# Performance work log

Hardware: AMD Instinct MI355X
Metric: run time of the kernel (lower is better)

Reference implementation:

```python
import jax, jax.numpy as jnp
import numpy as np

V, BLK, D, H, L = 50257, 2048, 768, 12, 4
HD = D // H
EPS = 1e-5


def _ln(x, w, b):
    mu = jnp.mean(x, axis=-1, keepdims=True)
    var = jnp.mean(jnp.square(x - mu), axis=-1, keepdims=True)
    return (x - mu) * jax.lax.rsqrt(var + EPS) * w + b


def setup_inputs() -> dict:
    key = jax.random.key(0)
    ks = iter(jax.random.split(key, 32))
    s = 0.02
    idx = jax.random.randint(next(ks), (2, 2048), 0, V)
    inp = {
        "idx": idx,
        "wte": jax.random.normal(next(ks), (V, D), jnp.float32) * s,
        "wpe": jax.random.normal(next(ks), (BLK, D), jnp.float32) * s,
        # stacked per-layer params [L, ...]
        "ln1_w": jnp.ones((L, D), jnp.float32),
        "ln1_b": jnp.zeros((L, D), jnp.float32),
        "attn_w": jax.random.normal(next(ks), (L, D, 3 * D), jnp.float32) * s,
        "attn_b": jnp.zeros((L, 3 * D), jnp.float32),
        "proj_w": jax.random.normal(next(ks), (L, D, D), jnp.float32) * (s / np.sqrt(2 * L)),
        "proj_b": jnp.zeros((L, D), jnp.float32),
        "ln2_w": jnp.ones((L, D), jnp.float32),
        "ln2_b": jnp.zeros((L, D), jnp.float32),
        "fc_w": jax.random.normal(next(ks), (L, D, 4 * D), jnp.float32) * s,
        "fc_b": jnp.zeros((L, 4 * D), jnp.float32),
        "fcp_w": jax.random.normal(next(ks), (L, 4 * D, D), jnp.float32) * (s / np.sqrt(2 * L)),
        "fcp_b": jnp.zeros((L, D), jnp.float32),
        "lnf_w": jnp.ones((D,), jnp.float32),
        "lnf_b": jnp.zeros((D,), jnp.float32),
    }
    return inp


def _gpt_forward(idx, wte, wpe, ln1_w, ln1_b, attn_w, attn_b, proj_w, proj_b,
                 ln2_w, ln2_b, fc_w, fc_b, fcp_w, fcp_b, lnf_w, lnf_b):
    B, T = idx.shape
    x = wte[idx] + wpe[:T]  # [B,T,D]; dropout p=0 -> identity
    causal = jnp.tril(jnp.ones((T, T), bool))
    scale = 1.0 / np.sqrt(HD)

    def block(x, p):
        l1w, l1b, aw, ab, pw, pb, l2w, l2b, fw, fb, fpw, fpb = p
        h = _ln(x, l1w, l1b)
        qkv = h @ aw + ab  # [B,T,3D]
        q, k, v = jnp.split(qkv, 3, axis=-1)
        q = q.reshape(B, T, H, HD).transpose(0, 2, 1, 3)  # [B,H,T,hd]
        k = k.reshape(B, T, H, HD).transpose(0, 2, 1, 3)
        v = v.reshape(B, T, H, HD).transpose(0, 2, 1, 3)
        att = jnp.einsum('bhqd,bhkd->bhqk', q, k) * scale
        att = jnp.where(causal, att, -jnp.inf)
        att = jax.nn.softmax(att, axis=-1)
        y = jnp.einsum('bhqk,bhkd->bhqd', att, v)
        y = y.transpose(0, 2, 1, 3).reshape(B, T, D)
        x = x + y @ pw + pb
        h2 = _ln(x, l2w, l2b)
        m = jax.nn.gelu(h2 @ fw + fb, approximate=False) @ fpw + fpb
        return x + m, None

    params = (ln1_w, ln1_b, attn_w, attn_b, proj_w, proj_b,
              ln2_w, ln2_b, fc_w, fc_b, fcp_w, fcp_b)
    x, _ = jax.lax.scan(block, x, params)
    x = _ln(x, lnf_w, lnf_b)
    # inference path: logits only for last position, lm_head tied to wte
    logits = x[:, -1:, :] @ wte.T  # [B,1,V]
    return logits


def reference(idx, wte, wpe, ln1_w, ln1_b, attn_w, attn_b, proj_w, proj_b,
              ln2_w, ln2_b, fc_w, fc_b, fcp_w, fcp_b, lnf_w, lnf_b):
    return _gpt_forward(idx, wte, wpe, ln1_w, ln1_b, attn_w, attn_b, proj_w, proj_b,
                        ln2_w, ln2_b, fc_w, fc_b, fcp_w, fcp_b, lnf_w, lnf_b)
```

## Files before the change

kernel.cpp:

```cpp
#include <hip/hip_runtime.h>
#include <math.h>

#define V 50257
#define B 2
#define T 2048
#define D 768
#define H 12
#define HD 64
#define L 4
#define D3 (3*D)
#define D4 (4*D)
#define NTOK (B*T)
#define EPS 1e-5f

typedef __bf16 v8bf __attribute__((ext_vector_type(8)));
typedef __bf16 v4bf __attribute__((ext_vector_type(4)));
typedef unsigned short v8us __attribute__((ext_vector_type(8)));
typedef float  v4f  __attribute__((ext_vector_type(4)));

#define GAS(p) ((const __attribute__((address_space(1))) void*)(p))
#define LAS(p) ((__attribute__((address_space(3))) void*)(p))

#define LIDX(row, chunk) ((row)*64 + ((((chunk) ^ ((row)&7)))<<3))
#define CIDX(row, chunk) ((row)*128 + ((((chunk) ^ ((row)&7)))<<3))

__global__ __launch_bounds__(256) void prep_kernel(
        const int* __restrict__ idx, const float* __restrict__ wte,
        const float* __restrict__ wpe, float* __restrict__ x,
        const float* __restrict__ aw_all,  const float* __restrict__ pw_all,
        const float* __restrict__ fw_all,  const float* __restrict__ fpw_all,
        __bf16* __restrict__ awt_all, __bf16* __restrict__ pwt_all,
        __bf16* __restrict__ fwt_all, __bf16* __restrict__ fpwt_all) {
    int bid = blockIdx.x;
    if (bid < 3072) {
        int e = (bid * 256 + threadIdx.x) * 4;
        int pos = e / D;
        int d   = e - pos * D;
        int t   = pos & (T - 1);
        int tok = idx[pos];
        const float4 a  = *(const float4*)(wte + (size_t)tok * D + d);
        const float4 p4 = *(const float4*)(wpe + (size_t)t * D + d);
        float4 r; r.x = a.x + p4.x; r.y = a.y + p4.y; r.z = a.z + p4.z; r.w = a.w + p4.w;
        *(float4*)(x + e) = r;
        return;
    }
    bid -= 3072;
    const int l = bid / 6912; bid -= l * 6912;
    const float* W; __bf16* Wt; int K, N, bx, by;
    if (bid < 1728)      {             W = aw_all  + (size_t)l * D  * D3; Wt = awt_all  + (size_t)l * D3 * D;  K = D;  N = D3; bx = bid % 72; by = bid / 72; }
    else if (bid < 2304) { bid -= 1728; W = pw_all  + (size_t)l * D  * D;  Wt = pwt_all  + (size_t)l * D  * D;  K = D;  N = D;  bx = bid % 24; by = bid / 24; }
    else if (bid < 4608) { bid -= 2304; W = fw_all  + (size_t)l * D  * D4; Wt = fwt_all  + (size_t)l * D4 * D;  K = D;  N = D4; bx = bid % 96; by = bid / 96; }
    else                 { bid -= 4608; W = fpw_all + (size_t)l * D4 * D;  Wt = fpwt_all + (size_t)l * D  * D4; K = D4; N = D;  bx = bid % 24; by = bid / 24; }
    __shared__ float t[32][33];
    const int n0 = bx * 32, k0 = by * 32;
    const int tx = threadIdx.x & 31, ty = threadIdx.x >> 5;
    #pragma unroll
    for (int p = 0; p < 4; ++p)
        t[ty + 8 * p][tx] = W[(size_t)(k0 + ty + 8 * p) * N + n0 + tx];
    __syncthreads();
    #pragma unroll
    for (int p = 0; p < 4; ++p)
        Wt[(size_t)(n0 + ty + 8 * p) * K + k0 + tx] = (__bf16)t[tx][ty + 8 * p];
}

__global__ __launch_bounds__(256) void ln_kernel(const float* __restrict__ X,
                                                 const float* __restrict__ w,
                                                 const float* __restrict__ b,
                                                 __bf16* __restrict__ Y,
                                                 int src_mul, int src_off) {
    int srow = blockIdx.x * src_mul + src_off;
    const float* xr = X + (size_t)srow * D;
    float v[3];
    float s = 0.f, s2 = 0.f;
    #pragma unroll
    for (int j = 0; j < 3; ++j) {
        v[j] = xr[threadIdx.x + 256 * j];
        s += v[j];
        s2 += v[j] * v[j];
    }
    #pragma unroll
    for (int off = 32; off; off >>= 1) {
        s  += __shfl_xor(s, off);
        s2 += __shfl_xor(s2, off);
    }
    __shared__ float ss[4], ss2[4];
    int wave = threadIdx.x >> 6, lane = threadIdx.x & 63;
    if (lane == 0) { ss[wave] = s; ss2[wave] = s2; }
    __syncthreads();
    s  = ss[0] + ss[1] + ss[2] + ss[3];
    s2 = ss2[0] + ss2[1] + ss2[2] + ss2[3];
    float mu  = s * (1.f / D);
    float var = s2 * (1.f / D) - mu * mu;
    float rs  = rsqrtf(var + EPS);
    __bf16* yr = Y + (size_t)blockIdx.x * D;
    #pragma unroll
    for (int j = 0; j < 3; ++j) {
        int c = threadIdx.x + 256 * j;
        yr[c] = (__bf16)((v[j] - mu) * rs * w[c] + b[c]);
    }
}

template<bool DOGELU>
__global__ __launch_bounds__(256) void gemm_bt(const __bf16* __restrict__ A,
                                               const __bf16* __restrict__ Wt,
                                               const float* __restrict__ bias,
                                               __bf16* __restrict__ Cout,
                                               int N, int K) {
    __shared__ __align__(16) __bf16 sm[16384];
    __bf16* As = sm;
    __bf16* Bs = sm + 8192;
    const int tid  = threadIdx.x;
    const int w    = tid >> 6;
    const int lane = tid & 63;
    const int row0 = blockIdx.y * 128;
    const int col0 = blockIdx.x * 128;

    const int srow = ((tid >> 6) & 3) * 16 + (tid & 15);
    const int sk   = ((tid >> 4) & 3) * 8;
    const __bf16* gA0 = A  + (size_t)(row0 + srow) * K + sk;
    const __bf16* gA1 = gA0 + (size_t)64 * K;
    const __bf16* gB0 = Wt + (size_t)(col0 + srow) * K + sk;
    const __bf16* gB1 = gB0 + (size_t)64 * K;
    __bf16* lA0 = As + (size_t)tid * 8;
    __bf16* lA1 = As + (size_t)(tid + 256) * 8;
    __bf16* lB0 = Bs + (size_t)tid * 8;
    __bf16* lB1 = Bs + (size_t)(tid + 256) * 8;

    const int wr = w >> 1, wc = w & 1;
    const __bf16* rA = As + wr * 2048 + lane * 8;
    const __bf16* rB = Bs + wc * 2048 + lane * 8;

    __builtin_amdgcn_global_load_lds(GAS(gA0), LAS(lA0), 16, 0, 0);
    __builtin_amdgcn_global_load_lds(GAS(gA1), LAS(lA1), 16, 0, 0);
    __builtin_amdgcn_global_load_lds(GAS(gB0), LAS(lB0), 16, 0, 0);
    __builtin_amdgcn_global_load_lds(GAS(gB1), LAS(lB1), 16, 0, 0);
    gA0 += 32; gA1 += 32; gB0 += 32; gB1 += 32;
    __syncthreads();

    v4f acc[4][4] = {};
    const int nt = K >> 5;
    for (int t = 0; t < nt; ++t) {
        const int cb = (t & 1) * 4096;
        if (t + 1 < nt) {
            const int nb = ((t + 1) & 1) * 4096;
            __builtin_amdgcn_global_load_lds(GAS(gA0), LAS(lA0 + nb), 16, 0, 0);
            __builtin_amdgcn_global_load_lds(GAS(gA1), LAS(lA1 + nb), 16, 0, 0);
            __builtin_amdgcn_global_load_lds(GAS(gB0), LAS(lB0 + nb), 16, 0, 0);
            __builtin_amdgcn_global_load_lds(GAS(gB1), LAS(lB1 + nb), 16, 0, 0);
            gA0 += 32; gA1 += 32; gB0 += 32; gB1 += 32;
        }
        v8bf af[4], bfr[4];
        #pragma unroll
        for (int i = 0; i < 4; ++i) af[i]  = *(const v8bf*)(rA + cb + i * 512);
        #pragma unroll
        for (int j = 0; j < 4; ++j) bfr[j] = *(const v8bf*)(rB + cb + j * 512);
        #pragma unroll
        for (int i = 0; i < 4; ++i)
            #pragma unroll
            for (int j = 0; j < 4; ++j)
                acc[i][j] = __builtin_amdgcn_mfma_f32_16x16x32_bf16(af[i], bfr[j], acc[i][j], 0, 0, 0);
        __syncthreads();
    }

    const int er = (lane >> 4) * 4;
    const int ec = lane & 15;
    #pragma unroll
    for (int j = 0; j < 4; ++j) {
        const int col = wc * 64 + j * 16 + ec;
        const float bval = bias[col0 + col];
        const int chunk = col >> 3, ce = col & 7;
        #pragma unroll
        for (int i = 0; i < 4; ++i) {
            const int rowb = wr * 64 + i * 16 + er;
            #pragma unroll
            for (int rr = 0; rr < 4; ++rr) {
                float vv = acc[i][j][rr] + bval;
                if (DOGELU) vv = 0.5f * vv * (1.f + erff(vv * 0.70710678118f));
                sm[CIDX(rowb + rr, chunk) + ce] = (__bf16)vv;
            }
        }
    }
    __syncthreads();
    #pragma unroll
    for (int c = 0; c < 8; ++c) {
        const int chunkid = tid + c * 256;
        const int row = chunkid >> 4;
        const int cc  = chunkid & 15;
        *(v8us*)(void*)(Cout + (size_t)(row0 + row) * N + col0 + cc * 8) =
            *(const v8us*)(const void*)(sm + CIDX(row, cc));
    }
}

__global__ __launch_bounds__(256) void gemm64(const __bf16* __restrict__ A,
                                              const __bf16* __restrict__ Wt,
                                              const float* __restrict__ bias,
                                              const float* __restrict__ res,
                                              float* __restrict__ Cout,
                                              int N, int K) {
    __shared__ __align__(16) __bf16 sm[16384];
    __bf16* As = sm;
    __bf16* Bs = sm + 8192;
    const int tid  = threadIdx.x;
    const int w    = tid >> 6;
    const int lane = tid & 63;
    const int row0 = blockIdx.y * 64;
    const int col0 = blockIdx.x * 64;

    const int srow = ((tid >> 7) & 3) * 16 + (tid & 15);
    const int sk   = ((tid >> 4) & 7) * 8;
    const __bf16* gA0 = A  + (size_t)(row0 + srow) * K + sk;
    const __bf16* gA1 = gA0 + (size_t)32 * K;
    const __bf16* gB0 = Wt + (size_t)(col0 + srow) * K + sk;
    const __bf16* gB1 = gB0 + (size_t)32 * K;
    __bf16* lA0 = As + (size_t)tid * 8;
    __bf16* lA1 = As + (size_t)(tid + 256) * 8;
    __bf16* lB0 = Bs + (size_t)tid * 8;
    __bf16* lB1 = Bs + (size_t)(tid + 256) * 8;

    const int wr = w >> 1, wc = w & 1;
    const __bf16* rA = As + wr * 2048 + lane * 8;
    const __bf16* rB = Bs + wc * 2048 + lane * 8;

    __builtin_amdgcn_global_load_lds(GAS(gA0), LAS(lA0), 16, 0, 0);
    __builtin_amdgcn_global_load_lds(GAS(gA1), LAS(lA1), 16, 0, 0);
    __builtin_amdgcn_global_load_lds(GAS(gB0), LAS(lB0), 16, 0, 0);
    __builtin_amdgcn_global_load_lds(GAS(gB1), LAS(lB1), 16, 0, 0);
    gA0 += 64; gA1 += 64; gB0 += 64; gB1 += 64;
    __syncthreads();

    v4f acc[2][2] = {};
    const int nt = K >> 6;
    for (int t = 0; t < nt; ++t) {
        const int cb = (t & 1) * 4096;
        if (t + 1 < nt) {
            const int nb = ((t + 1) & 1) * 4096;
            __builtin_amdgcn_global_load_lds(GAS(gA0), LAS(lA0 + nb), 16, 0, 0);
            __builtin_amdgcn_global_load_lds(GAS(gA1), LAS(lA1 + nb), 16, 0, 0);
            __builtin_amdgcn_global_load_lds(GAS(gB0), LAS(lB0 + nb), 16, 0, 0);
            __builtin_amdgcn_global_load_lds(GAS(gB1), LAS(lB1 + nb), 16, 0, 0);
            gA0 += 64; gA1 += 64; gB0 += 64; gB1 += 64;
        }
        #pragma unroll
        for (int h = 0; h < 2; ++h) {
            v8bf af[2], bfr[2];
            #pragma unroll
            for (int i = 0; i < 2; ++i) af[i]  = *(const v8bf*)(rA + cb + i * 1024 + h * 512);
            #pragma unroll
            for (int j = 0; j < 2; ++j) bfr[j] = *(const v8bf*)(rB + cb + j * 1024 + h * 512);
            #pragma unroll
            for (int i = 0; i < 2; ++i)
                #pragma unroll
                for (int j = 0; j < 2; ++j)
                    acc[i][j] = __builtin_amdgcn_mfma_f32_16x16x32_bf16(af[i], bfr[j], acc[i][j], 0, 0, 0);
        }
        __syncthreads();
    }

    const int er = (lane >> 4) * 4;
    const int ec = lane & 15;
    #pragma unroll
    for (int j = 0; j < 2; ++j) {
        const int col = col0 + wc * 32 + j * 16 + ec;
        const float bval = bias[col];
        #pragma unroll
        for (int i = 0; i < 2; ++i) {
            #pragma unroll
            for (int rr = 0; rr < 4; ++rr) {
                const int row = row0 + wr * 32 + i * 16 + er + rr;
                Cout[(size_t)row * N + col] = acc[i][j][rr] + bval + res[(size_t)row * N + col];
            }
        }
    }
}

__global__ __launch_bounds__(256) void attn_mfma(const __bf16* __restrict__ qkv,
                                                 __bf16* __restrict__ y) {
    __shared__ __align__(16) __bf16 Qs[4096];
    __shared__ __align__(16) __bf16 Ks[4096];
    __shared__ __align__(16) __bf16 Vt[4096];
    __shared__ __align__(16) __bf16 Ps[4][1024];

    const int tid  = threadIdx.x;
    const int w    = tid >> 6;
    const int lane = tid & 63;
    const int quad = lane >> 4;
    const int l4   = lane & 15;

    const int qt = 31 - (blockIdx.x & 31);
    const int bh = blockIdx.x >> 5;
    const int b  = bh / H;
    const int h  = bh - b * H;
    const int q0 = qt * 64;

    const __bf16* base = qkv + (size_t)(b * T) * D3 + h * HD;

    {
        int c = tid;
        #pragma unroll
        for (int rep = 0; rep < 2; ++rep, c += 256) {
            int row = c >> 3, ch = c & 7;
            v8us v = *(const v8us*)(const void*)(base + (size_t)(q0 + row) * D3 + ch * 8);
            *(v8us*)(void*)(Qs + LIDX(row, ch)) = v;
        }
    }

    const int krow = tid >> 3, kch = tid & 7;
    const int vkp = tid & 31, vdc = tid >> 5;
    const __bf16* kp0 = base + D     + (size_t)krow * D3 + kch * 8;
    const __bf16* kp1 = kp0 + (size_t)32 * D3;
    const __bf16* vp0 = base + 2 * D + (size_t)(2 * vkp) * D3 + vdc * 8;
    const __bf16* vp1 = vp0 + D3;

    v8us kr0 = *(const v8us*)(const void*)kp0;
    v8us kr1 = *(const v8us*)(const void*)kp1;
    v8us vr0 = *(const v8us*)(const void*)vp0;
    v8us vr1 = *(const v8us*)(const void*)vp1;

    float m_local = -INFINITY;
    v4f o[4] = {};
    v4f sacc = {};
    v8bf qf[2];
    v8bf vones;
    #pragma unroll
    for (int i = 0; i < 8; ++i) vones[i] = (__bf16)1.0f;

    const int nt = qt + 1;
    const size_t adv = (size_t)64 * D3;
    const int qrow = q0 + w * 16 + l4;

    for (int kt = 0; kt < nt; ++kt) {
        const int k0 = kt * 64;
        *(v8us*)(void*)(Ks + LIDX(krow, kch))      = kr0;
        *(v8us*)(void*)(Ks + LIDX(krow + 32, kch)) = kr1;
        #pragma unroll
        for (int j = 0; j < 8; ++j) {
            int dim = vdc * 8 + j;
            int idx = dim * 64 + ((((vkp >> 2) ^ (dim & 7))) << 3) + ((vkp & 3) << 1);
            *(unsigned int*)(void*)(Vt + idx) =
                ((unsigned int)vr1[j] << 16) | (unsigned int)vr0[j];
        }
        __syncthreads();

        if (kt == 0) {
            #pragma unroll
            for (int kh = 0; kh < 2; ++kh)
                qf[kh] = *(const v8bf*)(Qs + LIDX(w * 16 + l4, kh * 4 + quad));
        }
        if (kt + 1 < nt) {
            kp0 += adv; kp1 += adv; vp0 += adv; vp1 += adv;
            kr0 = *(const v8us*)(const void*)kp0;
            kr1 = *(const v8us*)(const void*)kp1;
            vr0 = *(const v8us*)(const void*)vp0;
            vr1 = *(const v8us*)(const void*)vp1;
        }

        v4f s[4] = {};
        __builtin_amdgcn_s_setprio(1);
        #pragma unroll
        for (int kh = 0; kh < 2; ++kh) {
            #pragma unroll
            for (int jb = 0; jb < 4; ++jb) {
                v8bf bk = *(const v8bf*)(Ks + LIDX(jb * 16 + l4, kh * 4 + quad));
                s[jb] = __builtin_amdgcn_mfma_f32_16x16x32_bf16(bk, qf[kh], s[jb], 0, 0, 0);
            }
        }
        __builtin_amdgcn_s_setprio(0);

        float sv[4][4];
        float mx = -INFINITY;
        #pragma unroll
        for (int jb = 0; jb < 4; ++jb) {
            #pragma unroll
            for (int rg = 0; rg < 4; ++rg) {
                float vvv = s[jb][rg] * 0.125f;
                if (k0 + jb * 16 + quad * 4 + rg > qrow) vvv = -INFINITY;
                sv[jb][rg] = vvv;
                mx = fmaxf(mx, vvv);
            }
        }
        mx = fmaxf(mx, __shfl_xor(mx, 16));
        mx = fmaxf(mx, __shfl_xor(mx, 32));
        if (!__all(mx <= m_local + 8.f)) {
            const float mnew    = fmaxf(m_local, mx);
            const float alpha_l = __expf(m_local - mnew);
            m_local = mnew;
            float a4[4];
            #pragma unroll
            for (int r = 0; r < 4; ++r) a4[r] = __shfl(alpha_l, quad * 4 + r);
            #pragma unroll
            for (int r = 0; r < 4; ++r) {
                sacc[r] *= a4[r];
                #pragma unroll
                for (int db = 0; db < 4; ++db) o[db][r] *= a4[r];
            }
        }
        #pragma unroll
        for (int jb = 0; jb < 4; ++jb) {
            v4bf pk;
            #pragma unroll
            for (int rg = 0; rg < 4; ++rg)
                pk[rg] = (__bf16)__expf(sv[jb][rg] - m_local);
            *(v4bf*)(void*)(&Ps[w][LIDX(l4, jb * 2 + (quad >> 1)) + ((quad & 1) << 2)]) = pk;
        }
        __builtin_amdgcn_s_setprio(1);
        #pragma unroll
        for (int kh = 0; kh < 2; ++kh) {
            v8bf ap = *(const v8bf*)(&Ps[w][LIDX(l4, kh * 4 + quad)]);
            sacc = __builtin_amdgcn_mfma_f32_16x16x32_bf16(ap, vones, sacc, 0, 0, 0);
            #pragma unroll
            for (int db = 0; db < 4; ++db) {
                v8bf bv = *(const v8bf*)(Vt + LIDX(db * 16 + l4, kh * 4 + quad));
                o[db] = __builtin_amdgcn_mfma_f32_16x16x32_bf16(ap, bv, o[db], 0, 0, 0);
            }
        }
        __builtin_amdgcn_s_setprio(0);
        __syncthreads();
    }

    #pragma unroll
    for (int db = 0; db < 4; ++db) {
        #pragma unroll
        for (int r = 0; r < 4; ++r) {
            const int q = q0 + w * 16 + quad * 4 + r;
            y[(size_t)(b * T + q) * D + h * HD + db * 16 + l4] =
                (__bf16)(o[db][r] / sacc[r]);
        }
    }
}

__global__ __launch_bounds__(256) void logits_kernel(const __bf16* __restrict__ xf,
                                                     const float* __restrict__ wte,
                                                     float* __restrict__ out) {
    int wave = threadIdx.x >> 6;
    int lane = threadIdx.x & 63;
    int v = blockIdx.x * 4 + wave;
    if (v >= V) return;
    const float4* wr = (const float4*)(wte + (size_t)v * D);
    const v4bf*   x0 = (const v4bf*)(xf);
    const v4bf*   x1 = (const v4bf*)(xf + D);
    float s0 = 0.f, s1 = 0.f;
    #pragma unroll
    for (int j = 0; j < 3; ++j) {
        float4 wv = wr[lane + 64 * j];
        v4bf a0 = x0[lane + 64 * j];
        v4bf a1 = x1[lane + 64 * j];
        s0 = fmaf(wv.x, (float)a0[0], s0); s0 = fmaf(wv.y, (float)a0[1], s0);
        s0 = fmaf(wv.z, (float)a0[2], s0); s0 = fmaf(wv.w, (float)a0[3], s0);
        s1 = fmaf(wv.x, (float)a1[0], s1); s1 = fmaf(wv.y, (float)a1[1], s1);
        s1 = fmaf(wv.z, (float)a1[2], s1); s1 = fmaf(wv.w, (float)a1[3], s1);
    }
    #pragma unroll
    for (int off = 32; off; off >>= 1) {
        s0 += __shfl_xor(s0, off);
        s1 += __shfl_xor(s1, off);
    }
    if (lane == 0) { out[v] = s0; out[V + v] = s1; }
}

extern "C" void kernel_launch(void* const* d_in, const int* in_sizes, int n_in,
                              void* d_out, int out_size, void* d_ws, size_t ws_size,
                              hipStream_t stream) {
    const int*   idx    = (const int*)  d_in[0];
    const float* wte    = (const float*)d_in[1];
    const float* wpe    = (const float*)d_in[2];
    const float* ln1_w  = (const float*)d_in[3];
    const float* ln1_b  = (const float*)d_in[4];
    const float* attn_w = (const float*)d_in[5];
    const float* attn_b = (const float*)d_in[6];
    const float* proj_w = (const float*)d_in[7];
    const float* proj_b = (const float*)d_in[8];
    const float* ln2_w  = (const float*)d_in[9];
    const float* ln2_b  = (const float*)d_in[10];
    const float* fc_w   = (const float*)d_in[11];
    const float* fc_b   = (const float*)d_in[12];
    const float* fcp_w  = (const float*)d_in[13];
    const float* fcp_b  = (const float*)d_in[14];
    const float* lnf_w  = (const float*)d_in[15];
    const float* lnf_b  = (const float*)d_in[16];
    float* out = (float*)d_out;

    char* ws = (char*)d_ws;
    float*  x    = (float*)ws;  ws += (size_t)NTOK * D  * 4;
    __bf16* qkvb = (__bf16*)ws;
    __bf16* gb   = (__bf16*)ws; ws += (size_t)NTOK * D4 * 2;
    __bf16* hb   = (__bf16*)ws; ws += (size_t)NTOK * D  * 2;
    __bf16* yb   = (__bf16*)ws; ws += (size_t)NTOK * D  * 2;
    __bf16* awt  = (__bf16*)ws; ws += (size_t)L * D3 * D   * 2;
    __bf16* pwt  = (__bf16*)ws; ws += (size_t)L * D  * D   * 2;
    __bf16* fwt  = (__bf16*)ws; ws += (size_t)L * D4 * D   * 2;
    __bf16* fpwt = (__bf16*)ws; ws += (size_t)L * D  * D4  * 2;
    __bf16* xf   = (__bf16*)ws; ws += (size_t)B * D    * 2;

    prep_kernel<<<3072 + 6912 * L, 256, 0, stream>>>(idx, wte, wpe, x,
                                                     attn_w, proj_w, fc_w, fcp_w,
                                                     awt, pwt, fwt, fpwt);

    for (int l = 0; l < L; ++l) {
        const float* l1w = ln1_w + l * D;
        const float* l1b = ln1_b + l * D;
        const float* ab  = attn_b + l * D3;
        const float* pb  = proj_b + l * D;
        const float* l2w = ln2_w + l * D;
        const float* l2b = ln2_b + l * D;
        const float* fb  = fc_b + l * D4;
        const float* fpb = fcp_b + l * D;
        const __bf16* awl  = awt  + (size_t)l * D3 * D;
        const __bf16* pwl  = pwt  + (size_t)l * D  * D;
        const __bf16* fwl  = fwt  + (size_t)l * D4 * D;
        const __bf16* fpwl = fpwt + (size_t)l * D  * D4;

        ln_kernel<<<NTOK, 256, 0, stream>>>(x, l1w, l1b, hb, 1, 0);
        gemm_bt<false><<<dim3(D3 / 128, NTOK / 128), 256, 0, stream>>>(
            hb, awl, ab, qkvb, D3, D);
        attn_mfma<<<B * H * (T / 64), 256, 0, stream>>>(qkvb, yb);
        gemm64<<<dim3(D / 64, NTOK / 64), 256, 0, stream>>>(
            yb, pwl, pb, x, x, D, D);
        ln_kernel<<<NTOK, 256, 0, stream>>>(x, l2w, l2b, hb, 1, 0);
        gemm_bt<true><<<dim3(D4 / 128, NTOK / 128), 256, 0, stream>>>(
            hb, fwl, fb, gb, D4, D);
        gemm64<<<dim3(D / 64, NTOK / 64), 256, 0, stream>>>(
            gb, fpwl, fpb, x, x, D, D4);
    }

    ln_kernel<<<B, 256, 0, stream>>>(x, lnf_w, lnf_b, xf, T, T - 1);
    logits_kernel<<<(V + 3) / 4, 256, 0, stream>>>(xf, wte, out);
}
```

Baseline: 1.286 ms.

## Triple-buffer GEMM loads, remap workgroups across XCDs, vectorize residual epilogue

Both GEMM kernels move from double to triple-buffered LDS staging, with explicit vmcnt waits and raw s_barriers so global-to-LDS loads run two tiles ahead. Workgroup IDs in the GEMMs and attention are permuted so consecutive tiles land on the same XCD, which is meant to improve L2 reuse. The gemm64 epilogue now stages results in swizzled LDS and writes float4 with coalesced residual reads. The cost is 1.5x LDS per block, which may reduce occupancy, plus correctness risk from the hand-written waitcnt counts.

```diff
diff --git a/kernel.cpp b/kernel.cpp
--- a/kernel.cpp
+++ b/kernel.cpp
@@ -23,6 +23,8 @@
 
 #define LIDX(row, chunk) ((row)*64 + ((((chunk) ^ ((row)&7)))<<3))
 #define CIDX(row, chunk) ((row)*128 + ((((chunk) ^ ((row)&7)))<<3))
+
+#define SBAR() asm volatile("s_barrier" ::: "memory")
 
 __global__ __launch_bounds__(256) void prep_kernel(
         const int* __restrict__ idx, const float* __restrict__ wte,
@@ -106,14 +108,16 @@
                                                const float* __restrict__ bias,
                                                __bf16* __restrict__ Cout,
                                                int N, int K) {
-    __shared__ __align__(16) __bf16 sm[16384];
-    __bf16* As = sm;
-    __bf16* Bs = sm + 8192;
+    __shared__ __align__(16) __bf16 sm[24576];
     const int tid  = threadIdx.x;
     const int w    = tid >> 6;
     const int lane = tid & 63;
-    const int row0 = blockIdx.y * 128;
-    const int col0 = blockIdx.x * 128;
+
+    int fid = blockIdx.y * gridDim.x + blockIdx.x;
+    const int nwg = gridDim.x * gridDim.y;
+    fid = (fid & 7) * (nwg >> 3) + (fid >> 3);
+    const int row0 = (fid / gridDim.x) * 128;
+    const int col0 = (fid % gridDim.x) * 128;
 
     const int srow = ((tid >> 6) & 3) * 16 + (tid & 15);
     const int sk   = ((tid >> 4) & 3) * 8;
@@ -121,33 +125,33 @@
     const __bf16* gA1 = gA0 + (size_t)64 * K;
     const __bf16* gB0 = Wt + (size_t)(col0 + srow) * K + sk;
     const __bf16* gB1 = gB0 + (size_t)64 * K;
-    __bf16* lA0 = As + (size_t)tid * 8;
-    __bf16* lA1 = As + (size_t)(tid + 256) * 8;
-    __bf16* lB0 = Bs + (size_t)tid * 8;
-    __bf16* lB1 = Bs + (size_t)(tid + 256) * 8;
+
+    auto stage = [&](int bsel) {
+        __bf16* dst = sm + bsel * 8192;
+        __builtin_amdgcn_global_load_lds(GAS(gA0), LAS(dst + (size_t)tid * 8), 16, 0, 0);
+        __builtin_amdgcn_global_load_lds(GAS(gA1), LAS(dst + (size_t)(tid + 256) * 8), 16, 0, 0);
+        __builtin_amdgcn_global_load_lds(GAS(gB0), LAS(dst + 4096 + (size_t)tid * 8), 16, 0, 0);
+        __builtin_amdgcn_global_load_lds(GAS(gB1), LAS(dst + 4096 + (size_t)(tid + 256) * 8), 16, 0, 0);
+        gA0 += 32; gA1 += 32; gB0 += 32; gB1 += 32;
+    };
 
     const int wr = w >> 1, wc = w & 1;
-    const __bf16* rA = As + wr * 2048 + lane * 8;
-    const __bf16* rB = Bs + wc * 2048 + lane * 8;
-
-    __builtin_amdgcn_global_load_lds(GAS(gA0), LAS(lA0), 16, 0, 0);
-    __builtin_amdgcn_global_load_lds(GAS(gA1), LAS(lA1), 16, 0, 0);
-    __builtin_amdgcn_global_load_lds(GAS(gB0), LAS(lB0), 16, 0, 0);
-    __builtin_amdgcn_global_load_lds(GAS(gB1), LAS(lB1), 16, 0, 0);
-    gA0 += 32; gA1 += 32; gB0 += 32; gB1 += 32;
-    __syncthreads();
+    const __bf16* rA = sm + wr * 2048 + lane * 8;
+    const __bf16* rB = sm + 4096 + wc * 2048 + lane * 8;
+
+    const int nt = K >> 5;
+    stage(0); stage(1);
 
     v4f acc[4][4] = {};
-    const int nt = K >> 5;
     for (int t = 0; t < nt; ++t) {
-        const int cb = (t & 1) * 4096;
-        if (t + 1 < nt) {
-            const int nb = ((t + 1) & 1) * 4096;
-            __builtin_amdgcn_global_load_lds(GAS(gA0), LAS(lA0 + nb), 16, 0, 0);
-            __builtin_amdgcn_global_load_lds(GAS(gA1), LAS(lA1 + nb), 16, 0, 0);
-            __builtin_amdgcn_global_load_lds(GAS(gB0), LAS(lB0 + nb), 16, 0, 0);
-            __builtin_amdgcn_global_load_lds(GAS(gB1), LAS(lB1 + nb), 16, 0, 0);
-            gA0 += 32; gA1 += 32; gB0 += 32; gB1 += 32;
+        const int cb = (t % 3) * 8192;
+        if (t + 2 < nt) {
+            stage((t + 2) % 3);
+            asm volatile("s_waitcnt vmcnt(8)\n\ts_barrier" ::: "memory");
+        } else if (t + 1 < nt) {
+            asm volatile("s_waitcnt vmcnt(4)\n\ts_barrier" ::: "memory");
+        } else {
+            asm volatile("s_waitcnt vmcnt(0)\n\ts_barrier" ::: "memory");
         }
         v8bf af[4], bfr[4];
         #pragma unroll
@@ -159,7 +163,7 @@
             #pragma unroll
             for (int j = 0; j < 4; ++j)
                 acc[i][j] = __builtin_amdgcn_mfma_f32_16x16x32_bf16(af[i], bfr[j], acc[i][j], 0, 0, 0);
-        __syncthreads();
+        SBAR();
     }
 
     const int er = (lane >> 4) * 4;
@@ -197,14 +201,16 @@
                                               const float* __restrict__ res,
                                               float* __restrict__ Cout,
                                               int N, int K) {
-    __shared__ __align__(16) __bf16 sm[16384];
-    __bf16* As = sm;
-    __bf16* Bs = sm + 8192;
+    __shared__ __align__(16) __bf16 sm[24576];
     const int tid  = threadIdx.x;
     const int w    = tid >> 6;
     const int lane = tid & 63;
-    const int row0 = blockIdx.y * 64;
-    const int col0 = blockIdx.x * 64;
+
+    int fid = blockIdx.y * gridDim.x + blockIdx.x;
+    const int nwg = gridDim.x * gridDim.y;
+    fid = (fid & 7) * (nwg >> 3) + (fid >> 3);
+    const int row0 = (fid / gridDim.x) * 64;
+    const int col0 = (fid % gridDim.x) * 64;
 
     const int srow = ((tid >> 7) & 3) * 16 + (tid & 15);
     const int sk   = ((tid >> 4) & 7) * 8;
@@ -212,33 +218,33 @@
     const __bf16* gA1 = gA0 + (size_t)32 * K;
     const __bf16* gB0 = Wt + (size_t)(col0 + srow) * K + sk;
     const __bf16* gB1 = gB0 + (size_t)32 * K;
-    __bf16* lA0 = As + (size_t)tid * 8;
-    __bf16* lA1 = As + (size_t)(tid + 256) * 8;
-    __bf16* lB0 = Bs + (size_t)tid * 8;
-    __bf16* lB1 = Bs + (size_t)(tid + 256) * 8;
+
+    auto stage = [&](int bsel) {
+        __bf16* dst = sm + bsel * 8192;
+        __builtin_amdgcn_global_load_lds(GAS(gA0), LAS(dst + (size_t)tid * 8), 16, 0, 0);
+        __builtin_amdgcn_global_load_lds(GAS(gA1), LAS(dst + (size_t)(tid + 256) * 8), 16, 0, 0);
+        __builtin_amdgcn_global_load_lds(GAS(gB0), LAS(dst + 4096 + (size_t)tid * 8), 16, 0, 0);
+        __builtin_amdgcn_global_load_lds(GAS(gB1), LAS(dst + 4096 + (size_t)(tid + 256) * 8), 16, 0, 0);
+        gA0 += 64; gA1 += 64; gB0 += 64; gB1 += 64;
+    };
 
     const int wr = w >> 1, wc = w & 1;
-    const __bf16* rA = As + wr * 2048 + lane * 8;
-    const __bf16* rB = Bs + wc * 2048 + lane * 8;
-
-    __builtin_amdgcn_global_load_lds(GAS(gA0), LAS(lA0), 16, 0, 0);
-    __builtin_amdgcn_global_load_lds(GAS(gA1), LAS(lA1), 16, 0, 0);
-    __builtin_amdgcn_global_load_lds(GAS(gB0), LAS(lB0), 16, 0, 0);
-    __builtin_amdgcn_global_load_lds(GAS(gB1), LAS(lB1), 16, 0, 0);
-    gA0 += 64; gA1 += 64; gB0 += 64; gB1 += 64;
-    __syncthreads();
+    const __bf16* rA = sm + wr * 2048 + lane * 8;
+    const __bf16* rB = sm + 4096 + wc * 2048 + lane * 8;
+
+    const int nt = K >> 6;
+    stage(0); stage(1);
 
     v4f acc[2][2] = {};
-    const int nt = K >> 6;
     for (int t = 0; t < nt; ++t) {
-        const int cb = (t & 1) * 4096;
-        if (t + 1 < nt) {
-            const int nb = ((t + 1) & 1) * 4096;
-            __builtin_amdgcn_global_load_lds(GAS(gA0), LAS(lA0 + nb), 16, 0, 0);
-            __builtin_amdgcn_global_load_lds(GAS(gA1), LAS(lA1 + nb), 16, 0, 0);
-            __builtin_amdgcn_global_load_lds(GAS(gB0), LAS(lB0 + nb), 16, 0, 0);
-            __builtin_amdgcn_global_load_lds(GAS(gB1), LAS(lB1 + nb), 16, 0, 0);
-            gA0 += 64; gA1 += 64; gB0 += 64; gB1 += 64;
+        const int cb = (t % 3) * 8192;
+        if (t + 2 < nt) {
+            stage((t + 2) % 3);
+            asm volatile("s_waitcnt vmcnt(8)\n\ts_barrier" ::: "memory");
+        } else if (t + 1 < nt) {
+            asm volatile("s_waitcnt vmcnt(4)\n\ts_barrier" ::: "memory");
+        } else {
+            asm volatile("s_waitcnt vmcnt(0)\n\ts_barrier" ::: "memory");
         }
         #pragma unroll
         for (int h = 0; h < 2; ++h) {
@@ -253,23 +259,35 @@
                 for (int j = 0; j < 2; ++j)
                     acc[i][j] = __builtin_amdgcn_mfma_f32_16x16x32_bf16(af[i], bfr[j], acc[i][j], 0, 0, 0);
         }
-        __syncthreads();
-    }
-
+        SBAR();
+    }
+
+    float* smf = (float*)sm;
     const int er = (lane >> 4) * 4;
     const int ec = lane & 15;
     #pragma unroll
     for (int j = 0; j < 2; ++j) {
-        const int col = col0 + wc * 32 + j * 16 + ec;
-        const float bval = bias[col];
+        const int col = wc * 32 + j * 16 + ec;
+        const float bval = bias[col0 + col];
         #pragma unroll
         for (int i = 0; i < 2; ++i) {
             #pragma unroll
             for (int rr = 0; rr < 4; ++rr) {
-                const int row = row0 + wr * 32 + i * 16 + er + rr;
-                Cout[(size_t)row * N + col] = acc[i][j][rr] + bval + res[(size_t)row * N + col];
+                const int row = wr * 32 + i * 16 + er + rr;
+                smf[row * 64 + (col ^ ((row & 3) << 4))] = acc[i][j][rr] + bval;
             }
         }
+    }
+    __syncthreads();
+    #pragma unroll
+    for (int c = 0; c < 4; ++c) {
+        const int chunkid = tid + c * 256;
+        const int row = chunkid >> 4;
+        const int c0  = (chunkid & 15) * 4;
+        float4 vv = *(const float4*)(smf + row * 64 + (c0 ^ ((row & 3) << 4)));
+        const float4 rv = *(const float4*)(res + (size_t)(row0 + row) * N + col0 + c0);
+        vv.x += rv.x; vv.y += rv.y; vv.z += rv.z; vv.w += rv.w;
+        *(float4*)(Cout + (size_t)(row0 + row) * N + col0 + c0) = vv;
     }
 }
 
@@ -286,8 +304,12 @@
     const int quad = lane >> 4;
     const int l4   = lane & 15;
 
-    const int qt = 31 - (blockIdx.x & 31);
-    const int bh = blockIdx.x >> 5;
+    int fid = blockIdx.x;
+    const int nwg = gridDim.x;
+    fid = (fid & 7) * (nwg >> 3) + (fid >> 3);
+
+    const int qt = 31 - (fid & 31);
+    const int bh = fid >> 5;
     const int b  = bh / H;
     const int h  = bh - b * H;
     const int q0 = qt * 64;
```

After: 1.265 ms. No clear change (-1.6%).
